# Kernel tuning notes

Hardware: AMD Instinct MI355X
Metric: run time of the kernel (lower is better)

## Reference

```python
import jax, jax.numpy as jnp
import numpy as np

TEMP = 1.0
EPS = 1e-15

B, N, F, K = 8, 2000, 128, 64


def setup_inputs() -> dict:
    key = jax.random.key(0)
    k1, k2, k3 = jax.random.split(key, 3)
    x = jax.random.normal(k1, (B, N, F), dtype=jnp.float32)
    adj = jax.random.uniform(k2, (B, N, N), dtype=jnp.float32)
    s = jax.random.normal(k3, (B, N, K), dtype=jnp.float32)
    mask = jnp.ones((B, N), dtype=bool)
    return {"x": x, "adj": adj, "s": s, "mask": mask}


def reference(x, adj, s, mask):
    k = s.shape[-1]
    s = jax.nn.softmax(s / TEMP, axis=-1)
    m = mask[..., None].astype(x.dtype)          # [B,N,1]
    x = x * m
    s = s * m

    # pooled features: s^T x -> [B,K,F]
    out = jnp.einsum('bnk,bnf->bkf', s, x)

    # pooled adjacency: s^T A s -> [B,K,K]
    as_ = jnp.einsum('bnm,bmk->bnk', adj, s)     # A s, [B,N,K]
    out_adj = jnp.einsum('bnk,bnl->bkl', as_, s)

    # mincut loss
    mincut_num = jnp.einsum('bkk->b', out_adj)
    d_flat = jnp.sum(adj, axis=-1)               # degree, [B,N]
    # trace(s^T diag(d) s) = sum_n d_n * sum_k s_nk^2 (avoids dense diag)
    mincut_den = jnp.einsum('bn,bnk,bnk->b', d_flat, s, s)
    mincut_loss = jnp.mean(-(mincut_num / mincut_den))

    # orthogonality loss
    ss = jnp.einsum('bnk,bnl->bkl', s, s)        # [B,K,K]
    ss_norm = jnp.linalg.norm(ss, axis=(-2, -1), keepdims=True)
    i_s = jnp.eye(k, dtype=ss.dtype)
    ortho = jnp.linalg.norm(ss / ss_norm - i_s / jnp.sqrt(jnp.asarray(k, ss.dtype)), axis=(-2, -1))
    ortho_loss = jnp.mean(ortho)

    # zero diagonal, symmetric degree normalization
    ind = jnp.arange(k)
    out_adj = out_adj.at[:, ind, ind].set(0.0)
    d = jnp.sqrt(jnp.sum(out_adj, axis=-1))[:, None, :] + EPS  # [B,1,K]
    out_adj = out_adj / d / jnp.swapaxes(d, 1, 2)

    return out, out_adj, mincut_loss, ortho_loss
```

## Files before the change

### kernel.cpp

```cpp
#include <hip/hip_runtime.h>

typedef __bf16 bf16;
typedef __bf16 bf16x4 __attribute__((ext_vector_type(4)));
typedef __bf16 bf16x8 __attribute__((ext_vector_type(8)));
typedef float f32x4 __attribute__((ext_vector_type(4)));

#define NB 8
#define NN 2000
#define N2 2048
#define KK 64
#define FF 128

__global__ __launch_bounds__(256) void k1_softmax(const float* __restrict__ s,
                                                  bf16* __restrict__ sT,
                                                  float* __restrict__ rowsq) {
  const int b = blockIdx.x >> 5, tile = blockIdx.x & 31;
  const int n0 = tile * 64;
  const int t = threadIdx.x;
  const int r = t >> 2, q = t & 3;
  __shared__ float ptile[64][65];
  const int n = n0 + r;
  const bool valid = n < NN;
  float v[16];
  if (valid) {
    const float4* src = (const float4*)(s + ((size_t)(b * NN + n)) * KK + q * 16);
#pragma unroll
    for (int i = 0; i < 4; ++i) {
      float4 f = src[i];
      v[4 * i + 0] = f.x; v[4 * i + 1] = f.y; v[4 * i + 2] = f.z; v[4 * i + 3] = f.w;
    }
  } else {
#pragma unroll
    for (int i = 0; i < 16; ++i) v[i] = 0.f;
  }
  float mx = v[0];
#pragma unroll
  for (int i = 1; i < 16; ++i) mx = fmaxf(mx, v[i]);
  mx = fmaxf(mx, __shfl_xor(mx, 1));
  mx = fmaxf(mx, __shfl_xor(mx, 2));
  float sum = 0.f;
#pragma unroll
  for (int i = 0; i < 16; ++i) { v[i] = __expf(v[i] - mx); sum += v[i]; }
  sum += __shfl_xor(sum, 1);
  sum += __shfl_xor(sum, 2);
  const float scale = valid ? (1.0f / sum) : 0.f;
  float rq = 0.f;
#pragma unroll
  for (int i = 0; i < 16; ++i) { v[i] *= scale; rq += v[i] * v[i]; }
  rq += __shfl_xor(rq, 1);
  rq += __shfl_xor(rq, 2);
  if (q == 0) rowsq[b * N2 + n0 + r] = rq;
#pragma unroll
  for (int i = 0; i < 16; ++i) ptile[r][q * 16 + i] = v[i];
  __syncthreads();
  bf16x8 o0, o1;
#pragma unroll
  for (int i = 0; i < 8; ++i) o0[i] = (bf16)ptile[q * 16 + i][r];
#pragma unroll
  for (int i = 0; i < 8; ++i) o1[i] = (bf16)ptile[q * 16 + 8 + i][r];
  bf16* dst = sT + ((size_t)(b * KK + r)) * N2 + n0 + q * 16;
  *(bf16x8*)dst = o0;
  *(bf16x8*)(dst + 8) = o1;
}

__device__ __forceinline__ bf16x8 cvt8(float4 a, float4 b) {
  bf16x8 v;
  v[0] = (bf16)a.x; v[1] = (bf16)a.y; v[2] = (bf16)a.z; v[3] = (bf16)a.w;
  v[4] = (bf16)b.x; v[5] = (bf16)b.y; v[6] = (bf16)b.z; v[7] = (bf16)b.w;
  return v;
}

__global__ __launch_bounds__(256) void k2_fused(const float* __restrict__ adj,
                                                const bf16* __restrict__ sT,
                                                const float* __restrict__ x,
                                                bf16* __restrict__ xT,
                                                bf16* __restrict__ asT,
                                                const float* __restrict__ rowsq,
                                                float* __restrict__ den_part) {
  __shared__ __align__(16) char smem[64 * 132 * 4];
  const int bid = blockIdx.x;
  const int t = threadIdx.x;

  if (bid >= 1024) {
    float* xt = (float*)smem;
    const int bb = (bid - 1024) >> 5, tl = (bid - 1024) & 31;
    const int n0b = tl * 64;
#pragma unroll
    for (int i = 0; i < 8; ++i) {
      int idx = t + 256 * i;
      int row = idx >> 5, c4 = idx & 31;
      int n = n0b + row;
      float4 vv = make_float4(0.f, 0.f, 0.f, 0.f);
      if (n < NN) vv = ((const float4*)(x + ((size_t)(bb * NN + n)) * FF))[c4];
      *(float4*)&xt[row * 132 + c4 * 4] = vv;
    }
    __syncthreads();
    const int f = t >> 1, h = t & 1;
    bf16* dst = xT + ((size_t)(bb * FF + f)) * N2 + n0b + h * 32;
#pragma unroll
    for (int g = 0; g < 4; ++g) {
      bf16x8 o;
#pragma unroll
      for (int i = 0; i < 8; ++i) o[i] = (bf16)xt[(h * 32 + g * 8 + i) * 132 + f];
      *(bf16x8*)(dst + g * 8) = o;
    }
    return;
  }

  const int b = bid >> 7, tile = bid & 127;
  if (tile >= 125) {
    if (tile == 125) {
      const int k = t >> 2, seg = t & 3;
      bf16x4 z = {(bf16)0.f, (bf16)0.f, (bf16)0.f, (bf16)0.f};
      bf16* p = asT + ((size_t)(b * KK + k)) * N2 + 2000 + seg * 12;
      *(bf16x4*)(p + 0) = z; *(bf16x4*)(p + 4) = z; *(bf16x4*)(p + 8) = z;
      if (t < 3) den_part[b * 128 + 125 + t] = 0.f;
    }
    return;
  }

  const int w = t >> 6, l = t & 63;
  const int lr = l & 15, lg = l >> 4;
  const int n0 = tile * 16;
  bf16* abuf = (bf16*)smem;
  float* dred = (float*)(smem + 8192);

  const int srow = t >> 4, scol = t & 15;
  const float* rowb = adj + ((size_t)(b * NN + n0 + srow)) * NN;
  bf16* wp = abuf + srow * 128 + ((scol ^ (srow & 7)) * 8);
  const bf16* sTw = sT + ((size_t)(b * KK + w * 16 + lr)) * N2;
  const bf16* arp = abuf + lr * 128;

  f32x4 acc;
#pragma unroll
  for (int r = 0; r < 4; ++r) acc[r] = 0.f;

  {
    const int mc = scol * 8;
    float4 A0 = *(const float4*)(rowb + mc);
    float4 A1 = *(const float4*)(rowb + mc + 4);
    *(bf16x8*)wp = cvt8(A0, A1);
  }

  for (int c = 0; c < 16; ++c) {
    __syncthreads();
    float4 A0, A1;
    if (c < 15) {
      int m1 = (c + 1) * 128 + scol * 8;
      int mc = m1 > 1992 ? 1992 : m1;
      A0 = *(const float4*)(rowb + mc);
      A1 = *(const float4*)(rowb + mc + 4);
    }
    const bf16* sTc = sTw + c * 128;
    const bf16* ac = arp + (c & 1) * 2048;
#pragma unroll
    for (int st = 0; st < 4; ++st) {
      bf16x8 bfrag = *(const bf16x8*)(sTc + st * 32 + lg * 8);
      bf16x8 afrag = *(const bf16x8*)(ac + (((st * 4 + lg) ^ (lr & 7)) * 8));
      acc = __builtin_amdgcn_mfma_f32_16x16x32_bf16(afrag, bfrag, acc, 0, 0, 0);
    }
    if (c < 15)
      *(bf16x8*)(wp + ((c + 1) & 1) * 2048) = cvt8(A0, A1);
  }

  bf16x4 o;
#pragma unroll
  for (int r = 0; r < 4; ++r) o[r] = (bf16)acc[r];
  *(bf16x4*)(asT + ((size_t)(b * KK + w * 16 + lr)) * N2 + n0 + lg * 4) = o;

  float s0 = acc[0], s1 = acc[1], s2 = acc[2], s3 = acc[3];
#pragma unroll
  for (int off = 1; off <= 8; off <<= 1) {
    s0 += __shfl_xor(s0, off); s1 += __shfl_xor(s1, off);
    s2 += __shfl_xor(s2, off); s3 += __shfl_xor(s3, off);
  }
  const float* rqp = rowsq + b * N2 + n0 + lg * 4;
  float part = s0 * rqp[0] + s1 * rqp[1] + s2 * rqp[2] + s3 * rqp[3];
  part += __shfl_xor(part, 16);
  part += __shfl_xor(part, 32);
  if (l == 0) dred[w] = part;
  __syncthreads();
  if (t == 0) den_part[b * 128 + tile] = dred[0] + dred[1] + dred[2] + dred[3];
}

__global__ __launch_bounds__(256) void k3_gemms(const bf16* __restrict__ sT,
                                                const bf16* __restrict__ asT,
                                                const bf16* __restrict__ xT,
                                                float* __restrict__ adjraw,
                                                float* __restrict__ ssw,
                                                float* __restrict__ dout) {
  const int b = blockIdx.x >> 6, u = blockIdx.x & 63;
  const bf16 *Ab, *Bb;
  float* Cb;
  int ldC;
  if (u < 16) {
    const int rt = u >> 2, ct = u & 3;
    Ab = asT + ((size_t)(b * KK + rt * 16)) * N2;
    Bb = sT + ((size_t)(b * KK + ct * 16)) * N2;
    Cb = adjraw + b * KK * KK + rt * 16 * KK + ct * 16; ldC = KK;
  } else if (u < 32) {
    const int v = u - 16, rt = v >> 2, ct = v & 3;
    Ab = sT + ((size_t)(b * KK + rt * 16)) * N2;
    Bb = sT + ((size_t)(b * KK + ct * 16)) * N2;
    Cb = ssw + b * KK * KK + rt * 16 * KK + ct * 16; ldC = KK;
  } else {
    const int v = u - 32, rt = v >> 3, ct = v & 7;
    Ab = sT + ((size_t)(b * KK + rt * 16)) * N2;
    Bb = xT + ((size_t)(b * FF + ct * 16)) * N2;
    Cb = dout + b * KK * FF + rt * 16 * FF + ct * 16; ldC = FF;
  }
  const int t = threadIdx.x;
  const int w = t >> 6, l = t & 63;
  const int lr = l & 15, lg = l >> 4;
  f32x4 acc;
#pragma unroll
  for (int r = 0; r < 4; ++r) acc[r] = 0.f;
  const int m_begin = w * 512;
#pragma unroll 4
  for (int s = 0; s < 16; ++s) {
    const int m = m_begin + s * 32 + lg * 8;
    bf16x8 af = *(const bf16x8*)(Ab + (size_t)lr * N2 + m);
    bf16x8 bfv = *(const bf16x8*)(Bb + (size_t)lr * N2 + m);
    acc = __builtin_amdgcn_mfma_f32_16x16x32_bf16(af, bfv, acc, 0, 0, 0);
  }
  __shared__ float red[4][16][16];
#pragma unroll
  for (int r = 0; r < 4; ++r) red[w][lg * 4 + r][lr] = acc[r];
  __syncthreads();
  const int row = t >> 4, col = t & 15;
  const float v = red[0][row][col] + red[1][row][col] +
                  red[2][row][col] + red[3][row][col];
  Cb[row * ldC + col] = v;
}

__device__ inline float wred64(float v) {
#pragma unroll
  for (int off = 32; off > 0; off >>= 1) v += __shfl_xor(v, off);
  return v;
}

__global__ __launch_bounds__(512) void k4_final(const float* __restrict__ adjraw,
                                                const float* __restrict__ ssw,
                                                const float* __restrict__ den_part,
                                                float* __restrict__ dout) {
  const int b = threadIdx.x >> 6;
  const int lane = threadIdx.x & 63;
  const float dp = den_part[b * 128 + lane] + den_part[b * 128 + 64 + lane];
  const float den = wred64(dp);
  const float* arow = adjraw + b * 4096 + lane * 64;
  float4 av[16];
#pragma unroll
  for (int i = 0; i < 16; ++i) av[i] = ((const float4*)arow)[i];
  const float diag = adjraw[b * 4096 + lane * 65];
  float rs = 0.f;
#pragma unroll
  for (int i = 0; i < 16; ++i) rs += av[i].x + av[i].y + av[i].z + av[i].w;
  rs -= diag;
  rs = fmaxf(rs, 0.f);
  const float num = wred64(diag);
  const float d = sqrtf(rs) + 1e-15f;
  __shared__ float dsh[8][64];
  __shared__ float lossm[8], losso[8];
  dsh[b][lane] = d;
  __syncthreads();
  const float invd = 1.0f / d;
  float* orow = dout + NB * KK * FF + b * 4096 + lane * 64;
#pragma unroll
  for (int i = 0; i < 16; ++i) {
    float4 cvv = av[i];
    cvv.x = (4 * i + 0 == lane) ? 0.f : cvv.x * invd / dsh[b][4 * i + 0];
    cvv.y = (4 * i + 1 == lane) ? 0.f : cvv.y * invd / dsh[b][4 * i + 1];
    cvv.z = (4 * i + 2 == lane) ? 0.f : cvv.z * invd / dsh[b][4 * i + 2];
    cvv.w = (4 * i + 3 == lane) ? 0.f : cvv.w * invd / dsh[b][4 * i + 3];
    ((float4*)orow)[i] = cvv;
  }
  const float* srow = ssw + b * 4096 + lane * 64;
  float4 sv[16];
  float sq = 0.f;
#pragma unroll
  for (int i = 0; i < 16; ++i) {
    sv[i] = ((const float4*)srow)[i];
    sq += sv[i].x * sv[i].x + sv[i].y * sv[i].y + sv[i].z * sv[i].z + sv[i].w * sv[i].w;
  }
  const float frob = sqrtf(wred64(sq));
  const float fi = 1.0f / frob;
  float osum = 0.f;
#pragma unroll
  for (int i = 0; i < 16; ++i) {
    float tx = sv[i].x * fi - ((4 * i + 0 == lane) ? 0.125f : 0.f);
    float ty = sv[i].y * fi - ((4 * i + 1 == lane) ? 0.125f : 0.f);
    float tz = sv[i].z * fi - ((4 * i + 2 == lane) ? 0.125f : 0.f);
    float tw = sv[i].w * fi - ((4 * i + 3 == lane) ? 0.125f : 0.f);
    osum += tx * tx + ty * ty + tz * tz + tw * tw;
  }
  const float ot = wred64(osum);
  if (lane == 0) {
    lossm[b] = -(num / den);
    losso[b] = sqrtf(ot);
  }
  __syncthreads();
  if (threadIdx.x == 0) {
    float m = 0.f, oo = 0.f;
#pragma unroll
    for (int b2 = 0; b2 < 8; ++b2) { m += lossm[b2]; oo += losso[b2]; }
    dout[NB * KK * FF + NB * KK * KK + 0] = m * 0.125f;
    dout[NB * KK * FF + NB * KK * KK + 1] = oo * 0.125f;
  }
}

extern "C" void kernel_launch(void* const* d_in, const int* in_sizes, int n_in,
                              void* d_out, int out_size, void* d_ws, size_t ws_size,
                              hipStream_t stream) {
  const float* x = (const float*)d_in[0];
  const float* adj = (const float*)d_in[1];
  const float* s = (const float*)d_in[2];
  float* out = (float*)d_out;
  char* ws = (char*)d_ws;
  bf16* sT = (bf16*)ws;
  bf16* xT = (bf16*)(ws + (2u << 20));
  bf16* asT = (bf16*)(ws + (6u << 20));
  float* rowsq = (float*)(ws + (8u << 20));
  float* den_part = (float*)(ws + (8u << 20) + 65536);
  float* adjraw = (float*)(ws + (8u << 20) + 65536 + 4096);
  float* ssw = adjraw + NB * KK * KK;

  k1_softmax<<<256, 256, 0, stream>>>(s, sT, rowsq);
  k2_fused<<<1280, 256, 0, stream>>>(adj, sT, x, xT, asT, rowsq, den_part);
  k3_gemms<<<512, 256, 0, stream>>>(sT, asT, xT, adjraw, ssw, out);
  k4_final<<<1, 512, 0, stream>>>(adjraw, ssw, den_part, out);
}
```

Measured before the change: 235.0 us.

## Stream adjacency tiles straight into LDS and split final reduction kernel

The adjacency GEMM kernel now uses global_load_lds to copy fp32 adjacency rows directly into swizzled, double-buffered LDS in 256-column chunks. The bf16 conversion moves to the fragment read just before each MFMA, replacing the register round-trip and the convert-then-store staging. The goal is to cut register pressure and load/store instruction overhead in the dominant memory-bound kernel, at the cost of twice the LDS traffic per element and a dependence on the barrier covering the async loads. The final kernel is also split into 8 per-batch blocks plus a tiny loss-averaging kernel, which adds one launch.

```diff
diff --git a/kernel.cpp b/kernel.cpp
--- a/kernel.cpp
+++ b/kernel.cpp
@@ -63,13 +63,6 @@
   *(bf16x8*)(dst + 8) = o1;
 }
 
-__device__ __forceinline__ bf16x8 cvt8(float4 a, float4 b) {
-  bf16x8 v;
-  v[0] = (bf16)a.x; v[1] = (bf16)a.y; v[2] = (bf16)a.z; v[3] = (bf16)a.w;
-  v[4] = (bf16)b.x; v[5] = (bf16)b.y; v[6] = (bf16)b.z; v[7] = (bf16)b.w;
-  return v;
-}
-
 __global__ __launch_bounds__(256) void k2_fused(const float* __restrict__ adj,
                                                 const bf16* __restrict__ sT,
                                                 const float* __restrict__ x,
@@ -77,12 +70,12 @@
                                                 bf16* __restrict__ asT,
                                                 const float* __restrict__ rowsq,
                                                 float* __restrict__ den_part) {
-  __shared__ __align__(16) char smem[64 * 132 * 4];
+  __shared__ __align__(16) float smf[64 * 132];
   const int bid = blockIdx.x;
   const int t = threadIdx.x;
 
   if (bid >= 1024) {
-    float* xt = (float*)smem;
+    float* xt = smf;
     const int bb = (bid - 1024) >> 5, tl = (bid - 1024) & 31;
     const int n0b = tl * 64;
 #pragma unroll
@@ -122,45 +115,51 @@
   const int w = t >> 6, l = t & 63;
   const int lr = l & 15, lg = l >> 4;
   const int n0 = tile * 16;
-  bf16* abuf = (bf16*)smem;
-  float* dred = (float*)(smem + 8192);
-
-  const int srow = t >> 4, scol = t & 15;
-  const float* rowb = adj + ((size_t)(b * NN + n0 + srow)) * NN;
-  bf16* wp = abuf + srow * 128 + ((scol ^ (srow & 7)) * 8);
+  float* dred = smf + 8192;
+
+  const float* adjb = adj + ((size_t)(b * NN + n0)) * NN;
   const bf16* sTw = sT + ((size_t)(b * KK + w * 16 + lr)) * N2;
-  const bf16* arp = abuf + lr * 128;
+  const int x7 = lr & 7;
 
   f32x4 acc;
 #pragma unroll
   for (int r = 0; r < 4; ++r) acc[r] = 0.f;
 
-  {
-    const int mc = scol * 8;
-    float4 A0 = *(const float4*)(rowb + mc);
-    float4 A1 = *(const float4*)(rowb + mc + 4);
-    *(bf16x8*)wp = cvt8(A0, A1);
-  }
-
-  for (int c = 0; c < 16; ++c) {
+#pragma unroll
+  for (int i = 0; i < 4; ++i) {
+    const int rr = (w << 2) + i;
+    int colf = (l ^ (rr & 7)) << 2;
+    if (colf > 1996) colf = 1996;
+    __builtin_amdgcn_global_load_lds(adjb + (size_t)rr * NN + colf,
+                                     &smf[rr * 256], 16, 0, 0);
+  }
+
+  for (int c = 0; c < 8; ++c) {
     __syncthreads();
-    float4 A0, A1;
-    if (c < 15) {
-      int m1 = (c + 1) * 128 + scol * 8;
-      int mc = m1 > 1992 ? 1992 : m1;
-      A0 = *(const float4*)(rowb + mc);
-      A1 = *(const float4*)(rowb + mc + 4);
-    }
-    const bf16* sTc = sTw + c * 128;
-    const bf16* ac = arp + (c & 1) * 2048;
-#pragma unroll
-    for (int st = 0; st < 4; ++st) {
+    if (c < 7) {
+      const int nb = (c + 1) & 1;
+#pragma unroll
+      for (int i = 0; i < 4; ++i) {
+        const int rr = (w << 2) + i;
+        int colf = (c + 1) * 256 + ((l ^ (rr & 7)) << 2);
+        if (colf > 1996) colf = 1996;
+        __builtin_amdgcn_global_load_lds(adjb + (size_t)rr * NN + colf,
+                                         &smf[nb * 4096 + rr * 256], 16, 0, 0);
+      }
+    }
+    const float* bufc = smf + (c & 1) * 4096 + lr * 256;
+    const bf16* sTc = sTw + c * 256;
+#pragma unroll
+    for (int st = 0; st < 8; ++st) {
       bf16x8 bfrag = *(const bf16x8*)(sTc + st * 32 + lg * 8);
-      bf16x8 afrag = *(const bf16x8*)(ac + (((st * 4 + lg) ^ (lr & 7)) * 8));
-      acc = __builtin_amdgcn_mfma_f32_16x16x32_bf16(afrag, bfrag, acc, 0, 0, 0);
-    }
-    if (c < 15)
-      *(bf16x8*)(wp + ((c + 1) & 1) * 2048) = cvt8(A0, A1);
+      const int g0 = st * 8 + lg * 2;
+      f32x4 a0 = *(const f32x4*)(bufc + ((g0 ^ x7) << 2));
+      f32x4 a1 = *(const f32x4*)(bufc + (((g0 + 1) ^ x7) << 2));
+      bf16x8 af;
+      af[0] = (bf16)a0[0]; af[1] = (bf16)a0[1]; af[2] = (bf16)a0[2]; af[3] = (bf16)a0[3];
+      af[4] = (bf16)a1[0]; af[5] = (bf16)a1[1]; af[6] = (bf16)a1[2]; af[7] = (bf16)a1[3];
+      acc = __builtin_amdgcn_mfma_f32_16x16x32_bf16(af, bfrag, acc, 0, 0, 0);
+    }
   }
 
   bf16x4 o;
@@ -239,12 +238,13 @@
   return v;
 }
 
-__global__ __launch_bounds__(512) void k4_final(const float* __restrict__ adjraw,
-                                                const float* __restrict__ ssw,
-                                                const float* __restrict__ den_part,
-                                                float* __restrict__ dout) {
-  const int b = threadIdx.x >> 6;
-  const int lane = threadIdx.x & 63;
+__global__ __launch_bounds__(64) void k4_final(const float* __restrict__ adjraw,
+                                               const float* __restrict__ ssw,
+                                               const float* __restrict__ den_part,
+                                               float* __restrict__ dout,
+                                               float* __restrict__ loss_part) {
+  const int b = blockIdx.x;
+  const int lane = threadIdx.x;
   const float dp = den_part[b * 128 + lane] + den_part[b * 128 + 64 + lane];
   const float den = wred64(dp);
   const float* arow = adjraw + b * 4096 + lane * 64;
@@ -259,19 +259,18 @@
   rs = fmaxf(rs, 0.f);
   const float num = wred64(diag);
   const float d = sqrtf(rs) + 1e-15f;
-  __shared__ float dsh[8][64];
-  __shared__ float lossm[8], losso[8];
-  dsh[b][lane] = d;
+  __shared__ float dsh[64];
+  dsh[lane] = d;
   __syncthreads();
   const float invd = 1.0f / d;
   float* orow = dout + NB * KK * FF + b * 4096 + lane * 64;
 #pragma unroll
   for (int i = 0; i < 16; ++i) {
     float4 cvv = av[i];
-    cvv.x = (4 * i + 0 == lane) ? 0.f : cvv.x * invd / dsh[b][4 * i + 0];
-    cvv.y = (4 * i + 1 == lane) ? 0.f : cvv.y * invd / dsh[b][4 * i + 1];
-    cvv.z = (4 * i + 2 == lane) ? 0.f : cvv.z * invd / dsh[b][4 * i + 2];
-    cvv.w = (4 * i + 3 == lane) ? 0.f : cvv.w * invd / dsh[b][4 * i + 3];
+    cvv.x = (4 * i + 0 == lane) ? 0.f : cvv.x * invd / dsh[4 * i + 0];
+    cvv.y = (4 * i + 1 == lane) ? 0.f : cvv.y * invd / dsh[4 * i + 1];
+    cvv.z = (4 * i + 2 == lane) ? 0.f : cvv.z * invd / dsh[4 * i + 2];
+    cvv.w = (4 * i + 3 == lane) ? 0.f : cvv.w * invd / dsh[4 * i + 3];
     ((float4*)orow)[i] = cvv;
   }
   const float* srow = ssw + b * 4096 + lane * 64;
@@ -295,16 +294,17 @@
   }
   const float ot = wred64(osum);
   if (lane == 0) {
-    lossm[b] = -(num / den);
-    losso[b] = sqrtf(ot);
-  }
-  __syncthreads();
-  if (threadIdx.x == 0) {
-    float m = 0.f, oo = 0.f;
-#pragma unroll
-    for (int b2 = 0; b2 < 8; ++b2) { m += lossm[b2]; oo += losso[b2]; }
+    loss_part[b] = -(num / den);
+    loss_part[8 + b] = sqrtf(ot);
+  }
+}
+
+__global__ void k5_loss(const float* __restrict__ loss_part, float* __restrict__ dout) {
+  if (threadIdx.x == 0 && blockIdx.x == 0) {
+    float m = 0.f, o = 0.f;
+    for (int b2 = 0; b2 < 8; ++b2) { m += loss_part[b2]; o += loss_part[8 + b2]; }
     dout[NB * KK * FF + NB * KK * KK + 0] = m * 0.125f;
-    dout[NB * KK * FF + NB * KK * KK + 1] = oo * 0.125f;
+    dout[NB * KK * FF + NB * KK * KK + 1] = o * 0.125f;
   }
 }
 
@@ -323,9 +323,11 @@
   float* den_part = (float*)(ws + (8u << 20) + 65536);
   float* adjraw = (float*)(ws + (8u << 20) + 65536 + 4096);
   float* ssw = adjraw + NB * KK * KK;
+  float* loss_part = ssw + NB * KK * KK;
 
   k1_softmax<<<256, 256, 0, stream>>>(s, sT, rowsq);
   k2_fused<<<1280, 256, 0, stream>>>(adj, sT, x, xT, asT, rowsq, den_part);
   k3_gemms<<<512, 256, 0, stream>>>(sT, asT, xT, adjraw, ssw, out);
-  k4_final<<<1, 512, 0, stream>>>(adjraw, ssw, den_part, out);
-}
+  k4_final<<<8, 64, 0, stream>>>(adjraw, ssw, den_part, out, loss_part);
+  k5_loss<<<1, 64, 0, stream>>>(loss_part, out);
+}
```

Measured after the change: 241.0 us. 1.03x slower.
